# Optimization experiments

Measured on AMD Instinct MI355X. Metric: run time of the kernel, lower is better.

The kernel has to match this reference:

```python
import jax, jax.numpy as jnp
import numpy as np

B = 64       # graphs per batch
n = 512      # nodes per graph (equal-size graphs)
F_IN = 128
F_HID = 128
F_OUT = 64
DEGREES = (2, 2)
AVG_DEG = 16


def setup_inputs() -> dict:
    key = jax.random.key(0)
    ks = jax.random.split(key, 12)
    N = B * n
    X = jax.random.normal(ks[0], (N, F_IN), dtype=jnp.float32)
    batch = jnp.repeat(jnp.arange(B, dtype=jnp.int64), n)
    # within-graph edges: a ring (guarantees no isolated nodes, so the
    # per-graph trimming in the original keeps all n nodes) + random edges
    E_rand = N * (AVG_DEG - 1)
    g = jax.random.randint(ks[1], (E_rand,), 0, B, dtype=jnp.int64)
    src_l = jax.random.randint(ks[2], (E_rand,), 0, n, dtype=jnp.int64)
    dst_l = jax.random.randint(ks[3], (E_rand,), 0, n, dtype=jnp.int64)
    src_r = jnp.arange(N, dtype=jnp.int64)
    dst_r = (src_r // n) * n + (src_r % n + 1) % n
    src = jnp.concatenate([g * n + src_l, src_r])
    dst = jnp.concatenate([g * n + dst_l, dst_r])
    edge_index = jnp.stack([src, dst])  # [2, 524288]
    xav = lambda k, sh: jax.random.normal(k, sh, dtype=jnp.float32) * np.sqrt(2.0 / (sh[-2] + sh[-1])).astype(np.float32)
    W1 = xav(ks[4], (DEGREES[0] + 1, F_IN, F_HID))
    b1 = jnp.zeros((F_HID,), jnp.float32)
    W2 = xav(ks[5], (DEGREES[1] + 1, F_HID, F_HID))
    b2 = jnp.zeros((F_HID,), jnp.float32)
    Wout = xav(ks[6], (F_HID, F_OUT))
    bout = jnp.zeros((F_OUT,), jnp.float32)
    alpha = jnp.float32(0.5)
    return {"X": X, "batch": batch, "edge_index": edge_index,
            "W1": W1, "b1": b1, "W2": W2, "b2": b2,
            "Wout": Wout, "bout": bout, "alpha": alpha}


def _conv(Xb, S, Ws, b):
    # out = sum_k S^k @ X @ W_k + b, then ReLU. Xb: [B,n,F], S: [B,n,n]
    out = jnp.einsum('bnf,fg->bng', Xb, Ws[0])
    Sx = Xb
    for k in range(1, Ws.shape[0]):
        Sx = jnp.einsum('bnm,bmf->bnf', S, Sx)
        out = out + jnp.einsum('bnf,fg->bng', Sx, Ws[k])
    return jax.nn.relu(out + b)


def reference(X, batch, edge_index, W1, b1, W2, b2, Wout, bout, alpha):
    src, dst = edge_index[0], edge_index[1]
    g = src // n  # edges are within-graph, so graph id from src
    # dense per-graph adjacency (== block-diag S of the original,
    # batched instead of one big [N,N] block-diagonal matrix)
    adj = jnp.zeros((B, n, n), jnp.float32).at[g, src % n, dst % n].add(1.0)
    S = alpha * adj + (1.0 - alpha) * jnp.eye(n, dtype=jnp.float32)
    x = X.reshape(B, n, -1)
    x = _conv(x, S, W1, b1)
    x = _conv(x, S, W2, b2)
    pooled = jnp.max(x, axis=1)          # global_max_pool -> [B, F_HID]
    return pooled @ Wout + bout          # [B, F_OUT]
```

## Files before the change

### kernel.cpp

```cpp
#include <hip/hip_runtime.h>
#include <hip/hip_bf16.h>

#define F 128
#define NG 512

typedef __attribute__((ext_vector_type(8))) short s16x8;
typedef __attribute__((ext_vector_type(4))) float f32x4;

__device__ inline float bf2f(unsigned short u) {
    unsigned int x = ((unsigned int)u) << 16;
    return __builtin_bit_cast(float, x);
}
__device__ inline unsigned short f2bf(float f) {
    __hip_bfloat16 h = __float2bfloat16(f);
    return __builtin_bit_cast(unsigned short, h);
}
__device__ inline unsigned int pack16(float x, float y) {
    return (unsigned int)f2bf(x) | ((unsigned int)f2bf(y) << 16);
}


__global__ __launch_bounds__(256) void prep_kernel(const float* __restrict__ X,
                                                   unsigned short* __restrict__ Xr,
                                                   unsigned short* __restrict__ Xc,
                                                   const float* __restrict__ W1,
                                                   const float* __restrict__ W2,
                                                   unsigned short* __restrict__ o1,
                                                   unsigned short* __restrict__ o2,
                                                   uint4* __restrict__ cntz) {
    __shared__ unsigned short tile[64][F + 4];
    int tid = threadIdx.x;
    if (blockIdx.x < 512) {
        int g = blockIdx.x >> 3;
        int nt = blockIdx.x & 7;
        int node0 = nt * 64;
        const float* Xg = X + ((size_t)g * NG + node0) * F;
        unsigned short* Xrg = Xr + ((size_t)g * NG + node0) * F;
        #pragma unroll
        for (int u = tid; u < 64 * 32; u += 256) {
            int row = u >> 5, c4 = u & 31;
            float4 v = ((const float4*)(Xg + (size_t)row * F))[c4];
            unsigned short a0 = f2bf(v.x), a1 = f2bf(v.y), a2 = f2bf(v.z), a3 = f2bf(v.w);
            tile[row][c4 * 4 + 0] = a0;
            tile[row][c4 * 4 + 1] = a1;
            tile[row][c4 * 4 + 2] = a2;
            tile[row][c4 * 4 + 3] = a3;
            uint2 w;
            w.x = (unsigned int)a0 | ((unsigned int)a1 << 16);
            w.y = (unsigned int)a2 | ((unsigned int)a3 << 16);
            ((uint2*)(Xrg + (size_t)row * F))[c4] = w;
        }
        __syncthreads();
        unsigned short* Xcg = Xc + (size_t)g * F * NG;
        #pragma unroll
        for (int u = tid; u < F * 16; u += 256) {
            int f = u >> 4, nb = u & 15;
            int n0 = nb * 4;
            uint2 w;
            w.x = (unsigned int)tile[n0 + 0][f] | ((unsigned int)tile[n0 + 1][f] << 16);
            w.y = (unsigned int)tile[n0 + 2][f] | ((unsigned int)tile[n0 + 3][f] << 16);
            ((uint2*)(Xcg + (size_t)f * NG + node0))[nb] = w;
        }
    } else if (blockIdx.x < 896) {
        int t = (blockIdx.x - 512) * 256 + tid;
        const float* W = (t < 49152) ? W1 : W2;
        unsigned short* o = (t < 49152) ? o1 : o2;
        int tt = (t < 49152) ? t : t - 49152;
        int j = tt & 7;
        int lane = (tt >> 3) & 63;
        int ct = (tt >> 9) & 7;
        int ks = tt >> 12;
        int k = ks * 32 + (lane >> 4) * 8 + j;
        int c = ct * 16 + (lane & 15);
        o[tt] = f2bf(W[(size_t)k * F + c]);
    } else {
        size_t base = (size_t)(blockIdx.x - 896) * 1024;
        uint4 z = {0u, 0u, 0u, 0u};
        #pragma unroll
        for (int i = 0; i < 4; ++i) cntz[base + i * 256 + tid] = z;
    }
}


__global__ void cnt_scatter_kernel(const int* __restrict__ src, const int* __restrict__ dst,
                                   unsigned int* __restrict__ cnt32, int E) {
    int e = blockIdx.x * blockDim.x + threadIdx.x;
    if (e >= E) return;
    int s = src[e], d = dst[e];
    size_t idx = ((size_t)s << 9) | (unsigned)(d & (NG - 1));
    atomicAdd(&cnt32[idx >> 2], 1u << ((idx & 3) * 8));
}

__global__ __launch_bounds__(256) void sgen_kernel(const unsigned char* __restrict__ cnt,
                                                   unsigned short* __restrict__ Sb,
                                                   const float* __restrict__ alphap) {
    size_t t = (size_t)blockIdx.x * 256 + threadIdx.x;
    size_t base = t * 8;
    float alpha = *alphap;
    float diag = 1.0f - alpha;
    int i = (int)((base >> 9) & (NG - 1));
    int j0 = (int)(base & (NG - 1));
    uint2 c = *(const uint2*)(cnt + base);
    unsigned short o[8];
    #pragma unroll
    for (int b = 0; b < 8; ++b) {
        unsigned cv = ((b < 4) ? (c.x >> (8 * b)) : (c.y >> (8 * (b - 4)))) & 0xffu;
        float v = alpha * (float)cv + ((i == j0 + b) ? diag : 0.f);
        o[b] = f2bf(v);
    }
    uint4 w;
    w.x = (unsigned int)o[0] | ((unsigned int)o[1] << 16);
    w.y = (unsigned int)o[2] | ((unsigned int)o[3] << 16);
    w.z = (unsigned int)o[4] | ((unsigned int)o[5] << 16);
    w.w = (unsigned int)o[6] | ((unsigned int)o[7] << 16);
    *(uint4*)(Sb + base) = w;
}


__global__ __launch_bounds__(512) void sapply_kernel(
    const unsigned short* __restrict__ S, const unsigned short* __restrict__ Bc,
    unsigned short* __restrict__ Cr, unsigned short* __restrict__ Cc) {
    __shared__ unsigned short Bs[65536];
    const int g = blockIdx.x >> 2, rt = blockIdx.x & 3;
    const int tid = threadIdx.x, wave = tid >> 6, lane = tid & 63;
    const int l15 = lane & 15, hi = lane >> 4;
    const int lrow = wave * 16 + l15;

    const unsigned short* Bcg = Bc + (size_t)g * F * NG;
    #pragma unroll
    for (int it = 0; it < 16; ++it) {
        int u = it * 512 + tid;
        int f = u >> 6, c = u & 63;
        *(uint4*)(Bs + f * 512 + ((c ^ (f & 7)) << 3)) =
            *(const uint4*)(Bcg + (size_t)f * NG + (c << 3));
    }
    __syncthreads();

    f32x4 acc[8];
    #pragma unroll
    for (int ct = 0; ct < 8; ++ct) acc[ct] = (f32x4){0.f, 0.f, 0.f, 0.f};

    const unsigned short* Sg = S + ((size_t)g * NG + rt * 128 + lrow) * NG;
    const int bxor = l15 & 7;
    #pragma unroll 4
    for (int ks = 0; ks < 16; ++ks) {
        s16x8 a = *(const s16x8*)(Sg + ks * 32 + hi * 8);
        #pragma unroll
        for (int ct = 0; ct < 8; ++ct) {
            int col = ct * 16 + l15;
            s16x8 b = *(const s16x8*)(Bs + col * 512 + ((((ks << 2) | hi) ^ bxor) << 3));
            acc[ct] = __builtin_amdgcn_mfma_f32_16x16x32_bf16(a, b, acc[ct], 0, 0, 0);
        }
    }
    __syncthreads();

    const int rloc = wave * 16 + (hi << 2);
    unsigned short* OutS = Bs + 40960;
    unsigned short* Ccg = Cc + (size_t)g * F * NG + rt * 128 + rloc;
    #pragma unroll
    for (int ct = 0; ct < 8; ++ct) {
        int col = ct * 16 + l15;
        uint2 w;
        w.x = pack16(acc[ct][0], acc[ct][1]);
        w.y = pack16(acc[ct][2], acc[ct][3]);
        *(uint2*)(Ccg + (size_t)col * NG) = w;
        #pragma unroll
        for (int r = 0; r < 4; ++r)
            OutS[(rloc + r) * F + col] = f2bf(acc[ct][r]);
    }
    __syncthreads();
    uint4* o4 = (uint4*)(Cr + ((size_t)g * NG + rt * 128) * F);
    const uint4* s4 = (const uint4*)OutS;
    #pragma unroll
    for (int u = tid; u < 128 * F / 8; u += 512) o4[u] = s4[u];
}


template <int WRITE_H>
__global__ __launch_bounds__(512) void fused_conv_kernel(
    const unsigned short* __restrict__ S, const unsigned short* __restrict__ Bc,
    const unsigned short* __restrict__ A0, const unsigned short* __restrict__ A1,
    const unsigned short* __restrict__ Wswz, const float* __restrict__ bias,
    unsigned short* __restrict__ Hr, unsigned short* __restrict__ Hc,
    float* __restrict__ pooledp) {
    __shared__ unsigned short Bs[65536];
    const int g = blockIdx.x >> 2, rt = blockIdx.x & 3;
    const int tid = threadIdx.x, wave = tid >> 6, lane = tid & 63;
    const int l15 = lane & 15, hi = lane >> 4;
    const int lrow = wave * 16 + l15;

    const unsigned short* Bcg = Bc + (size_t)g * F * NG;
    #pragma unroll
    for (int it = 0; it < 16; ++it) {
        int u = it * 512 + tid;
        int f = u >> 6, c = u & 63;
        *(uint4*)(Bs + f * 512 + ((c ^ (f & 7)) << 3)) =
            *(const uint4*)(Bcg + (size_t)f * NG + (c << 3));
    }
    __syncthreads();

    f32x4 sacc[8];
    #pragma unroll
    for (int ct = 0; ct < 8; ++ct) sacc[ct] = (f32x4){0.f, 0.f, 0.f, 0.f};
    {
        const unsigned short* Sg = S + ((size_t)g * NG + rt * 128 + lrow) * NG;
        const int bxor = l15 & 7;
        #pragma unroll 4
        for (int ks = 0; ks < 16; ++ks) {
            s16x8 a = *(const s16x8*)(Sg + ks * 32 + hi * 8);
            #pragma unroll
            for (int ct = 0; ct < 8; ++ct) {
                int col = ct * 16 + l15;
                s16x8 b = *(const s16x8*)(Bs + col * 512 + ((((ks << 2) | hi) ^ bxor) << 3));
                sacc[ct] = __builtin_amdgcn_mfma_f32_16x16x32_bf16(a, b, sacc[ct], 0, 0, 0);
            }
        }
    }
    __syncthreads();

    {
        int rloc = wave * 16 + (hi << 2);
        #pragma unroll
        for (int ct = 0; ct < 8; ++ct) {
            int col = ct * 16 + l15;
            #pragma unroll
            for (int r = 0; r < 4; ++r)
                Bs[(rloc + r) * 136 + col] = f2bf(sacc[ct][r]);
        }
    }
    __syncthreads();

    f32x4 acc[8];
    #pragma unroll
    for (int ct = 0; ct < 8; ++ct) acc[ct] = (f32x4){0.f, 0.f, 0.f, 0.f};
    const int arow = blockIdx.x * 128 + lrow;
    #pragma unroll
    for (int ks = 0; ks < 12; ++ks) {
        s16x8 a;
        if (ks < 4) {
            a = *(const s16x8*)(A0 + (size_t)arow * F + ks * 32 + hi * 8);
        } else if (ks < 8) {
            a = *(const s16x8*)(A1 + (size_t)arow * F + (ks - 4) * 32 + hi * 8);
        } else {
            a = *(const s16x8*)(Bs + lrow * 136 + (ks - 8) * 32 + hi * 8);
        }
        const unsigned short* wb = Wswz + ((size_t)ks * 512 + lane) * 8;
        #pragma unroll
        for (int ct = 0; ct < 8; ++ct) {
            s16x8 b = *(const s16x8*)(wb + (size_t)ct * 512);
            acc[ct] = __builtin_amdgcn_mfma_f32_16x16x32_bf16(a, b, acc[ct], 0, 0, 0);
        }
    }

    const int rloc = wave * 16 + (hi << 2);
    if (WRITE_H) {
        unsigned short* OutS = Bs + 40960;
        #pragma unroll
        for (int ct = 0; ct < 8; ++ct) {
            int col = ct * 16 + l15;
            float b = bias[col];
            float v0 = fmaxf(acc[ct][0] + b, 0.f);
            float v1 = fmaxf(acc[ct][1] + b, 0.f);
            float v2 = fmaxf(acc[ct][2] + b, 0.f);
            float v3 = fmaxf(acc[ct][3] + b, 0.f);
            uint2 w;
            w.x = pack16(v0, v1);
            w.y = pack16(v2, v3);
            *(uint2*)(Hc + (size_t)g * F * NG + (size_t)col * NG + rt * 128 + rloc) = w;
            OutS[(rloc + 0) * F + col] = f2bf(v0);
            OutS[(rloc + 1) * F + col] = f2bf(v1);
            OutS[(rloc + 2) * F + col] = f2bf(v2);
            OutS[(rloc + 3) * F + col] = f2bf(v3);
        }
        __syncthreads();
        uint4* o4 = (uint4*)(Hr + ((size_t)g * NG + rt * 128) * F);
        const uint4* s4 = (const uint4*)OutS;
        #pragma unroll
        for (int u = tid; u < 128 * F / 8; u += 512) o4[u] = s4[u];
    } else {
        __syncthreads();
        float* wmax = (float*)Bs;
        #pragma unroll
        for (int ct = 0; ct < 8; ++ct) {
            int col = ct * 16 + l15;
            float b = bias[col];
            float m = fmaxf(fmaxf(acc[ct][0], acc[ct][1]), fmaxf(acc[ct][2], acc[ct][3]));
            m = fmaxf(m + b, 0.f);
            m = fmaxf(m, __shfl_xor(m, 16));
            m = fmaxf(m, __shfl_xor(m, 32));
            if (lane < 16) wmax[wave * F + col] = m;
        }
        __syncthreads();
        if (tid < F) {
            float m = wmax[tid];
            #pragma unroll
            for (int w = 1; w < 8; ++w) m = fmaxf(m, wmax[w * F + tid]);
            pooledp[((size_t)rt * 64 + g) * F + tid] = m;
        }
    }
}


__global__ __launch_bounds__(64) void out_gemm_kernel(const float* __restrict__ pooledp,
                                                      const float* __restrict__ Wout,
                                                      const float* __restrict__ bout,
                                                      float* __restrict__ out) {
    __shared__ float p[F];
    int b = blockIdx.x, t = threadIdx.x;
    #pragma unroll
    for (int c = t; c < F; c += 64) {
        float m = pooledp[(size_t)b * F + c];
        m = fmaxf(m, pooledp[((size_t)64 + b) * F + c]);
        m = fmaxf(m, pooledp[((size_t)128 + b) * F + c]);
        m = fmaxf(m, pooledp[((size_t)192 + b) * F + c]);
        p[c] = m;
    }
    __syncthreads();
    float acc = bout[t];
    #pragma unroll 8
    for (int k = 0; k < F; ++k) acc += p[k] * Wout[k * 64 + t];
    out[(size_t)b * 64 + t] = acc;
}


extern "C" void kernel_launch(void* const* d_in, const int* in_sizes, int n_in,
                              void* d_out, int out_size, void* d_ws, size_t ws_size,
                              hipStream_t stream) {
    const float* X     = (const float*)d_in[0];
    const int*   ei    = (const int*)d_in[2];
    const float* W1    = (const float*)d_in[3];
    const float* b1    = (const float*)d_in[4];
    const float* W2    = (const float*)d_in[5];
    const float* b2    = (const float*)d_in[6];
    const float* Wout  = (const float*)d_in[7];
    const float* bout  = (const float*)d_in[8];
    const float* alpha = (const float*)d_in[9];

    const int N = in_sizes[0] / F;
    const int E = in_sizes[2] / 2;
    const int Bg = N / NG;

    const int* srcv = ei;
    const int* dstv = ei + E;

    char* ws = (char*)d_ws;
    const size_t SBYTES = (size_t)Bg * NG * NG * 2;
    const size_t PBYTES = (size_t)N * F * 2;

    unsigned short* Sb = (unsigned short*)ws;
    unsigned short* P0 = (unsigned short*)(ws + SBYTES);
    unsigned short* P1 = (unsigned short*)(ws + SBYTES + PBYTES);
    unsigned short* P2 = (unsigned short*)(ws + SBYTES + 2 * PBYTES);
    unsigned short* P3 = (unsigned short*)(ws + SBYTES + 3 * PBYTES);
    char* tail = ws + SBYTES + 4 * PBYTES;
    unsigned short* Wswz1 = (unsigned short*)tail;
    unsigned short* Wswz2 = Wswz1 + (size_t)3 * F * F;
    float* pooledp = (float*)(Wswz2 + (size_t)3 * F * F);
    unsigned int* cnt32 = (unsigned int*)P2;

    prep_kernel<<<1920, 256, 0, stream>>>(X, P0, P1, W1, W2, Wswz1, Wswz2, (uint4*)cnt32);

    cnt_scatter_kernel<<<(E + 255) / 256, 256, 0, stream>>>(srcv, dstv, cnt32, E);
    sgen_kernel<<<(Bg * NG * NG / 8) / 256, 256, 0, stream>>>((const unsigned char*)cnt32, Sb, alpha);

    sapply_kernel<<<Bg * 4, 512, 0, stream>>>(Sb, P1, P2, P3);
    fused_conv_kernel<1><<<Bg * 4, 512, 0, stream>>>(Sb, P3, P0, P2, Wswz1, b1, P0, P1, nullptr);

    sapply_kernel<<<Bg * 4, 512, 0, stream>>>(Sb, P1, P2, P3);
    fused_conv_kernel<0><<<Bg * 4, 512, 0, stream>>>(Sb, P3, P0, P2, Wswz2, b2, nullptr, nullptr, pooledp);

    out_gemm_kernel<<<Bg, 64, 0, stream>>>(pooledp, Wout, bout, (float*)d_out);
}
```

Measured before the change: 137.1 us.

## Fuse adjacency generation into GEMM kernels, reading 8-bit counts directly

Removes the separate sgen kernel that expanded the 8-bit edge-count matrix into a bf16 S matrix. The sapply and fused_conv kernels now load uint8 counts and build the bf16 A fragments on the fly as alpha*count plus the diagonal term. This drops one kernel launch and one full write of S (32 MB), and halves the bytes each of the four GEMM passes reads for S. The cost is extra per-fragment ALU conversion work inside the MFMA loop, and the count buffer now lives in its own workspace region instead of aliasing P2.

```diff
diff --git a/kernel.cpp b/kernel.cpp
--- a/kernel.cpp
+++ b/kernel.cpp
@@ -17,6 +17,19 @@
 }
 __device__ inline unsigned int pack16(float x, float y) {
     return (unsigned int)f2bf(x) | ((unsigned int)f2bf(y) << 16);
+}
+
+__device__ inline s16x8 sfrag(const unsigned char* __restrict__ crow, int kbase, int row,
+                              float alpha, float diagv) {
+    uint2 b8 = *(const uint2*)(crow + kbase);
+    s16x8 a;
+    #pragma unroll
+    for (int j = 0; j < 8; ++j) {
+        unsigned bj = ((j < 4) ? (b8.x >> (8 * j)) : (b8.y >> (8 * (j - 4)))) & 0xffu;
+        float v = alpha * (float)bj + ((kbase + j) == row ? diagv : 0.f);
+        a[j] = (short)f2bf(v);
+    }
+    return a;
 }
 
 
@@ -91,40 +104,19 @@
     atomicAdd(&cnt32[idx >> 2], 1u << ((idx & 3) * 8));
 }
 
-__global__ __launch_bounds__(256) void sgen_kernel(const unsigned char* __restrict__ cnt,
-                                                   unsigned short* __restrict__ Sb,
-                                                   const float* __restrict__ alphap) {
-    size_t t = (size_t)blockIdx.x * 256 + threadIdx.x;
-    size_t base = t * 8;
-    float alpha = *alphap;
-    float diag = 1.0f - alpha;
-    int i = (int)((base >> 9) & (NG - 1));
-    int j0 = (int)(base & (NG - 1));
-    uint2 c = *(const uint2*)(cnt + base);
-    unsigned short o[8];
-    #pragma unroll
-    for (int b = 0; b < 8; ++b) {
-        unsigned cv = ((b < 4) ? (c.x >> (8 * b)) : (c.y >> (8 * (b - 4)))) & 0xffu;
-        float v = alpha * (float)cv + ((i == j0 + b) ? diag : 0.f);
-        o[b] = f2bf(v);
-    }
-    uint4 w;
-    w.x = (unsigned int)o[0] | ((unsigned int)o[1] << 16);
-    w.y = (unsigned int)o[2] | ((unsigned int)o[3] << 16);
-    w.z = (unsigned int)o[4] | ((unsigned int)o[5] << 16);
-    w.w = (unsigned int)o[6] | ((unsigned int)o[7] << 16);
-    *(uint4*)(Sb + base) = w;
-}
-
 
 __global__ __launch_bounds__(512) void sapply_kernel(
-    const unsigned short* __restrict__ S, const unsigned short* __restrict__ Bc,
+    const unsigned char* __restrict__ cnt, const float* __restrict__ alphap,
+    const unsigned short* __restrict__ Bc,
     unsigned short* __restrict__ Cr, unsigned short* __restrict__ Cc) {
     __shared__ unsigned short Bs[65536];
     const int g = blockIdx.x >> 2, rt = blockIdx.x & 3;
     const int tid = threadIdx.x, wave = tid >> 6, lane = tid & 63;
     const int l15 = lane & 15, hi = lane >> 4;
     const int lrow = wave * 16 + l15;
+    const int row = rt * 128 + lrow;
+    const float alpha = *alphap;
+    const float diagv = 1.0f - alpha;
 
     const unsigned short* Bcg = Bc + (size_t)g * F * NG;
     #pragma unroll
@@ -140,11 +132,11 @@
     #pragma unroll
     for (int ct = 0; ct < 8; ++ct) acc[ct] = (f32x4){0.f, 0.f, 0.f, 0.f};
 
-    const unsigned short* Sg = S + ((size_t)g * NG + rt * 128 + lrow) * NG;
+    const unsigned char* crow = cnt + ((size_t)g * NG + row) * NG;
     const int bxor = l15 & 7;
     #pragma unroll 4
     for (int ks = 0; ks < 16; ++ks) {
-        s16x8 a = *(const s16x8*)(Sg + ks * 32 + hi * 8);
+        s16x8 a = sfrag(crow, ks * 32 + hi * 8, row, alpha, diagv);
         #pragma unroll
         for (int ct = 0; ct < 8; ++ct) {
             int col = ct * 16 + l15;
@@ -178,7 +170,8 @@
 
 template <int WRITE_H>
 __global__ __launch_bounds__(512) void fused_conv_kernel(
-    const unsigned short* __restrict__ S, const unsigned short* __restrict__ Bc,
+    const unsigned char* __restrict__ cnt, const float* __restrict__ alphap,
+    const unsigned short* __restrict__ Bc,
     const unsigned short* __restrict__ A0, const unsigned short* __restrict__ A1,
     const unsigned short* __restrict__ Wswz, const float* __restrict__ bias,
     unsigned short* __restrict__ Hr, unsigned short* __restrict__ Hc,
@@ -188,6 +181,9 @@
     const int tid = threadIdx.x, wave = tid >> 6, lane = tid & 63;
     const int l15 = lane & 15, hi = lane >> 4;
     const int lrow = wave * 16 + l15;
+    const int row = rt * 128 + lrow;
+    const float alpha = *alphap;
+    const float diagv = 1.0f - alpha;
 
     const unsigned short* Bcg = Bc + (size_t)g * F * NG;
     #pragma unroll
@@ -203,11 +199,11 @@
     #pragma unroll
     for (int ct = 0; ct < 8; ++ct) sacc[ct] = (f32x4){0.f, 0.f, 0.f, 0.f};
     {
-        const unsigned short* Sg = S + ((size_t)g * NG + rt * 128 + lrow) * NG;
+        const unsigned char* crow = cnt + ((size_t)g * NG + row) * NG;
         const int bxor = l15 & 7;
         #pragma unroll 4
         for (int ks = 0; ks < 16; ++ks) {
-            s16x8 a = *(const s16x8*)(Sg + ks * 32 + hi * 8);
+            s16x8 a = sfrag(crow, ks * 32 + hi * 8, row, alpha, diagv);
             #pragma unroll
             for (int ct = 0; ct < 8; ++ct) {
                 int col = ct * 16 + l15;
@@ -344,30 +340,28 @@
     const int* dstv = ei + E;
 
     char* ws = (char*)d_ws;
-    const size_t SBYTES = (size_t)Bg * NG * NG * 2;
+    const size_t CBYTES = (size_t)Bg * NG * NG;
     const size_t PBYTES = (size_t)N * F * 2;
 
-    unsigned short* Sb = (unsigned short*)ws;
-    unsigned short* P0 = (unsigned short*)(ws + SBYTES);
-    unsigned short* P1 = (unsigned short*)(ws + SBYTES + PBYTES);
-    unsigned short* P2 = (unsigned short*)(ws + SBYTES + 2 * PBYTES);
-    unsigned short* P3 = (unsigned short*)(ws + SBYTES + 3 * PBYTES);
-    char* tail = ws + SBYTES + 4 * PBYTES;
+    unsigned char* cnt8 = (unsigned char*)ws;
+    unsigned short* P0 = (unsigned short*)(ws + CBYTES);
+    unsigned short* P1 = (unsigned short*)(ws + CBYTES + PBYTES);
+    unsigned short* P2 = (unsigned short*)(ws + CBYTES + 2 * PBYTES);
+    unsigned short* P3 = (unsigned short*)(ws + CBYTES + 3 * PBYTES);
+    char* tail = ws + CBYTES + 4 * PBYTES;
     unsigned short* Wswz1 = (unsigned short*)tail;
     unsigned short* Wswz2 = Wswz1 + (size_t)3 * F * F;
     float* pooledp = (float*)(Wswz2 + (size_t)3 * F * F);
-    unsigned int* cnt32 = (unsigned int*)P2;
-
-    prep_kernel<<<1920, 256, 0, stream>>>(X, P0, P1, W1, W2, Wswz1, Wswz2, (uint4*)cnt32);
-
-    cnt_scatter_kernel<<<(E + 255) / 256, 256, 0, stream>>>(srcv, dstv, cnt32, E);
-    sgen_kernel<<<(Bg * NG * NG / 8) / 256, 256, 0, stream>>>((const unsigned char*)cnt32, Sb, alpha);
-
-    sapply_kernel<<<Bg * 4, 512, 0, stream>>>(Sb, P1, P2, P3);
-    fused_conv_kernel<1><<<Bg * 4, 512, 0, stream>>>(Sb, P3, P0, P2, Wswz1, b1, P0, P1, nullptr);
-
-    sapply_kernel<<<Bg * 4, 512, 0, stream>>>(Sb, P1, P2, P3);
-    fused_conv_kernel<0><<<Bg * 4, 512, 0, stream>>>(Sb, P3, P0, P2, Wswz2, b2, nullptr, nullptr, pooledp);
+
+    prep_kernel<<<1920, 256, 0, stream>>>(X, P0, P1, W1, W2, Wswz1, Wswz2, (uint4*)cnt8);
+
+    cnt_scatter_kernel<<<(E + 255) / 256, 256, 0, stream>>>(srcv, dstv, (unsigned int*)cnt8, E);
+
+    sapply_kernel<<<Bg * 4, 512, 0, stream>>>(cnt8, alpha, P1, P2, P3);
+    fused_conv_kernel<1><<<Bg * 4, 512, 0, stream>>>(cnt8, alpha, P3, P0, P2, Wswz1, b1, P0, P1, nullptr);
+
+    sapply_kernel<<<Bg * 4, 512, 0, stream>>>(cnt8, alpha, P1, P2, P3);
+    fused_conv_kernel<0><<<Bg * 4, 512, 0, stream>>>(cnt8, alpha, P3, P0, P2, Wswz2, b2, nullptr, nullptr, pooledp);
 
     out_gemm_kernel<<<Bg, 64, 0, stream>>>(pooledp, Wout, bout, (float*)d_out);
 }
```

Result: faster. 127.9 us (-6.8%).
